# Performance work log

Hardware: AMD Instinct MI355X
Metric: run time of the kernel (lower is better)

The kernel has to match this reference:

```python
import jax, jax.numpy as jnp
import numpy as np

DIST = 3.0
COEFF = 10.0
NEG_SLOPE = 0.3  # keras LeakyReLU default


def _probe_points(dist=DIST):
    # fixed 26 probe offsets on a sphere of radius `dist` (from build())
    angles = np.array(
        [[j * 0.125 - 0.125, i * 0.125 + (j - 1) * 0.0625] for j in range(3) for i in range(8)]
        + [[-0.25, 0.0], [0.25, 0.0]],
        dtype=np.float32,
    ) * (2.0 * np.pi)
    a, b = angles[:, 0], angles[:, 1]
    pts = np.stack([np.sin(a), np.cos(a) * np.cos(b), np.cos(a) * np.sin(b)], axis=-1) * dist
    return jnp.asarray(pts, dtype=jnp.float32)  # (26, 3)


def setup_inputs() -> dict:
    key = jax.random.key(0)
    k1, k2, k3 = jax.random.split(key, 3)
    B, n, f = 2, 1024, 3
    m, out_feats, num_convs = 26, 6, 5
    points = jax.random.normal(k1, (B, n, 3 + f), dtype=jnp.float32)
    # per-conv Dense(m*f -> out_feats) weights/bias, stacked over num_convs
    W = jax.random.normal(k2, (num_convs, m * f, out_feats), dtype=jnp.float32) * 0.1
    b = jax.random.normal(k3, (num_convs, out_feats), dtype=jnp.float32) * 0.1
    return {"points": points, "W": W, "b": b}


def reference(points, W, b):
    B, n, df = points.shape
    d = 3
    f = df - d
    probes = _probe_points()              # (m, d)
    m = probes.shape[0]
    coords = points[..., :d]              # (B, n, d) -> centers too (l = n)
    feats = points[..., d:]               # (B, n, f)
    centers = coords
    # probes per center: (B, l, m, d)
    probes_per_center = centers[:, :, None, :] + probes[None, None, :, :]
    # delta: (B, l, m, n, d)
    delta = coords[:, None, None, :, :] - probes_per_center[:, :, :, None, :]
    sq = jnp.sum(delta * delta, axis=-1)  # (B, l, m, n)
    wgt = COEFF / (sq + COEFF)            # inverse-distance weights
    # weighted feature sum: (B, l, m, f), averaged over n
    wf = jnp.einsum('blmn,bnf->blmf', wgt, feats) / n
    x = wf.reshape(B, n, m * f)           # (B, l, m*f)
    # num_convs parallel Dense + LeakyReLU (Dropout is identity at inference)
    h = jnp.einsum('blx,kxo->blko', x, W) + b[None, None, :, :]
    h = jnp.where(h > 0, h, NEG_SLOPE * h)
    convs = h.reshape(B, n, -1)           # (B, n, num_convs*out_feats)
    return jnp.concatenate([centers, convs], axis=-1)  # (B, n, 3 + 30)
```

## Files before the change

kernel.cpp:

```cpp
#include <hip/hip_runtime.h>


#define NPTS   1024
#define COEFF  10.0f
#define NEG    0.3f

typedef float  v2f __attribute__((ext_vector_type(2)));
typedef __fp16 h2  __attribute__((ext_vector_type(2)));

#define CA 4.24264068f
#define CY 3.91968890f
#define CZ 1.62358830f

constexpr int M0[14] = {0,5, 1,4, 2,3, 7,6, 8,12, 10,14, 24,25};
constexpr int M1[12] = {16,19, 17,18, 20,23, 21,22, 9,13, 11,15};

__device__ __forceinline__ v2f vfma(float c, v2f a, v2f b) {
#if __has_builtin(__builtin_elementwise_fma)
  return __builtin_elementwise_fma(v2f{c, c}, a, b);
#else
  return v2f{fmaf(c, a.x, b.x), fmaf(c, a.y, b.y)};
#endif
}

#define DPP_STEP(x, ctrl, rm, bm, bc)                                        \
  x += __int_as_float(__builtin_amdgcn_update_dpp(                           \
      0, __float_as_int(x), ctrl, rm, bm, bc))

__device__ __forceinline__ float wave_sum_to_lane63(float x) {
  DPP_STEP(x, 0x111, 0xf, 0xf, true);
  DPP_STEP(x, 0x112, 0xf, 0xf, true);
  DPP_STEP(x, 0x114, 0xf, 0xe, false);
  DPP_STEP(x, 0x118, 0xf, 0xc, false);
  DPP_STEP(x, 0x142, 0xa, 0xf, false);
  DPP_STEP(x, 0x143, 0xc, 0xf, false);
  return x;
}

template <int HALF>
__device__ __forceinline__ void tgen(v2f dx, v2f dy, v2f dz, v2f base, v2f* t) {
  if constexpr (HALF == 0) {
    const v2f rx = vfma( CA, dx, base);
    const v2f sA = vfma( CZ, dz, rx);
    const v2f sB = vfma(-CZ, dz, rx);
    const v2f sC = vfma(-CY, dz, rx);
    const v2f sD = vfma( CY, dz, rx);
    t[0]  = vfma(-CY, dy, sA);   t[1]  = vfma( CY, dy, sA);
    t[2]  = vfma(-CY, dy, sB);   t[3]  = vfma( CY, dy, sB);
    t[4]  = vfma(-CZ, dy, sC);   t[5]  = vfma( CZ, dy, sC);
    t[6]  = vfma(-CZ, dy, sD);   t[7]  = vfma( CZ, dy, sD);
    t[8]  = vfma(-6.f, dy, base); t[9]  = vfma( 6.f, dy, base);
    t[10] = vfma(-6.f, dz, base); t[11] = vfma( 6.f, dz, base);
    t[12] = vfma( 6.f, dx, base); t[13] = vfma(-6.f, dx, base);
  } else {
    const v2f rx = vfma(-CA, dx, base);
    const v2f sA = vfma(-CZ, dz, rx);
    const v2f sB = vfma(-CY, dz, rx);
    const v2f sC = vfma( CZ, dz, rx);
    const v2f sD = vfma( CY, dz, rx);
    const v2f u = dy + dz, v = dy - dz;
    t[0]  = vfma(-CY, dy, sA);   t[1]  = vfma( CY, dy, sA);
    t[2]  = vfma(-CZ, dy, sB);   t[3]  = vfma( CZ, dy, sB);
    t[4]  = vfma( CY, dy, sC);   t[5]  = vfma(-CY, dy, sC);
    t[6]  = vfma( CZ, dy, sD);   t[7]  = vfma(-CZ, dy, sD);
    t[8]  = vfma(-CA, u, base);  t[9]  = vfma( CA, u, base);
    t[10] = vfma( CA, v, base);  t[11] = vfma(-CA, v, base);
  }
}

template <int HALF>
__device__ void run_main(const float* __restrict__ batch, int lane,
                         float cx, float cy, float cz, float* acc) {
  constexpr int NP = HALF ? 12 : 14;
  for (int it = 0; it < NPTS / 128; ++it) {
    const float* prowA = batch + (it * 128 + lane) * 6;
    const float* prowB = prowA + 64 * 6;
    const float2 a0 = *reinterpret_cast<const float2*>(prowA);
    const float2 a1 = *reinterpret_cast<const float2*>(prowA + 2);
    const float2 a2 = *reinterpret_cast<const float2*>(prowA + 4);
    const float2 b0 = *reinterpret_cast<const float2*>(prowB);
    const float2 b1 = *reinterpret_cast<const float2*>(prowB + 2);
    const float2 b2 = *reinterpret_cast<const float2*>(prowB + 4);

    const v2f dx = v2f{a0.x, b0.x} - cx;
    const v2f dy = v2f{a0.y, b0.y} - cy;
    const v2f dz = v2f{a1.x, b1.x} - cz;
    v2f base = vfma(1.f, dz * dz, v2f{19.f, 19.f});
    base = __builtin_elementwise_fma(dy, dy, base);
    base = __builtin_elementwise_fma(dx, dx, base);

    v2f t[NP];
    tgen<HALF>(dx, dy, dz, base, t);

    const h2 f0p = __builtin_amdgcn_cvt_pkrtz(a1.y, b1.y);
    const h2 f1p = __builtin_amdgcn_cvt_pkrtz(a2.x, b2.x);
    const h2 f2p = __builtin_amdgcn_cvt_pkrtz(a2.y, b2.y);

    #pragma unroll
    for (int j = 0; j < NP; ++j) {
      const float r  = __builtin_amdgcn_rcpf(t[j].x * t[j].y);
      const h2 wp = __builtin_amdgcn_cvt_pkrtz(t[j].y * r, t[j].x * r);
      acc[j * 3 + 0] = __builtin_amdgcn_fdot2(wp, f0p, acc[j * 3 + 0], false);
      acc[j * 3 + 1] = __builtin_amdgcn_fdot2(wp, f1p, acc[j * 3 + 1], false);
      acc[j * 3 + 2] = __builtin_amdgcn_fdot2(wp, f2p, acc[j * 3 + 2], false);
    }
  }
}

template <int HALF>
__device__ __forceinline__ void reduce_store(float* acc, int lane, float* sx) {
  constexpr int NP = HALF ? 12 : 14;
  #pragma unroll
  for (int j = 0; j < NP * 3; ++j)
    acc[j] = wave_sum_to_lane63(acc[j]);
  if (lane == 63) {
    #pragma unroll
    for (int j = 0; j < NP; ++j) {
      const int m = HALF ? M1[j] : M0[j];
      sx[m * 3 + 0] = acc[j * 3 + 0];
      sx[m * 3 + 1] = acc[j * 3 + 1];
      sx[m * 3 + 2] = acc[j * 3 + 2];
    }
  }
}

__global__ __launch_bounds__(256, 4) void crossconv_kernel(
    const float* __restrict__ points,
    const float* __restrict__ W,
    const float* __restrict__ bias,
    float* __restrict__ out)
{
    __shared__ __align__(16) float sx[2][80];

    const int tid    = threadIdx.x;
    const int lane   = tid & 63;
    const int w      = tid >> 6;
    const int cLocal = w >> 1;
    const int half   = w & 1;
    const int G      = blockIdx.x * 2 + cLocal;

    const float* batch = points + (G >> 10) * (NPTS * 6);
    const float* crow  = points + G * 6;
    const float  cx = crow[0], cy = crow[1], cz = crow[2];

    float acc[42];
    #pragma unroll
    for (int j = 0; j < 42; ++j) acc[j] = 0.f;

    if (half == 0) run_main<0>(batch, lane, cx, cy, cz, acc);
    else           run_main<1>(batch, lane, cx, cy, cz, acc);

    if (half == 0) reduce_store<0>(acc, lane, sx[cLocal]);
    else           reduce_store<1>(acc, lane, sx[cLocal]);
    __syncthreads();

    if (half == 0) {
      const float scale = COEFF / (float)NPTS;
      float* orow = out + G * 33;
      if (lane < 30) {
        const int k = lane / 6, o = lane % 6;
        const float* Wk = W + k * (78 * 6) + o;
        float h0 = 0.f, h1 = 0.f, h2_ = 0.f, h3 = 0.f;
        const float4* sxv = reinterpret_cast<const float4*>(sx[cLocal]);
        #pragma unroll
        for (int t4 = 0; t4 < 19; ++t4) {
          const float4 v = sxv[t4];
          h0  = fmaf(v.x, Wk[(t4 * 4 + 0) * 6], h0);
          h1  = fmaf(v.y, Wk[(t4 * 4 + 1) * 6], h1);
          h2_ = fmaf(v.z, Wk[(t4 * 4 + 2) * 6], h2_);
          h3  = fmaf(v.w, Wk[(t4 * 4 + 3) * 6], h3);
        }
        const float2 vt = *reinterpret_cast<const float2*>(&sx[cLocal][76]);
        h0 = fmaf(vt.x, Wk[76 * 6], h0);
        h1 = fmaf(vt.y, Wk[77 * 6], h1);
        const float dot = (h0 + h2_) + (h1 + h3);
        float h = fmaf(dot, scale, bias[lane]);
        h = (h > 0.f) ? h : NEG * h;
        orow[3 + lane] = h;
      } else if (lane < 33) {
        orow[lane - 30] = (lane == 30) ? cx : ((lane == 31) ? cy : cz);
      }
    }
}

extern "C" void kernel_launch(void* const* d_in, const int* in_sizes, int n_in,
                              void* d_out, int out_size, void* d_ws, size_t ws_size,
                              hipStream_t stream) {
    const float* points = (const float*)d_in[0];
    const float* W      = (const float*)d_in[1];
    const float* bias   = (const float*)d_in[2];
    float* out          = (float*)d_out;
    crossconv_kernel<<<1024, 256, 0, stream>>>(points, W, bias, out);
}
```

Measured before the change: 23.69 us.

## Batch reciprocals across probes, force packed FP32 asm, and reduce in packed fp16

Replaces the per-probe reciprocal with a batched product trick, so one v_rcp serves four probe pairs (eight weights) at the cost of extra multiplies. The probe-distance FMAs are now inline-asm v_pk_fma_f32/v_pk_add_f32 with neg modifiers, so they are guaranteed to issue as packed ops. The final cross-lane DPP reduction converts accumulator pairs to packed fp16 and sums them as h2, halving the DPP steps. Risks: products of up to eight t values may overflow or lose precision in fp32, and summing 64 lanes in fp16 cuts reduction accuracy.

Measured after the change: 23.82 us. Within noise of the previous version (+0.5%).

```diff
diff --git a/kernel.cpp b/kernel.cpp
--- a/kernel.cpp
+++ b/kernel.cpp
@@ -15,63 +15,75 @@
 constexpr int M0[14] = {0,5, 1,4, 2,3, 7,6, 8,12, 10,14, 24,25};
 constexpr int M1[12] = {16,19, 17,18, 20,23, 21,22, 9,13, 11,15};
 
-__device__ __forceinline__ v2f vfma(float c, v2f a, v2f b) {
-#if __has_builtin(__builtin_elementwise_fma)
-  return __builtin_elementwise_fma(v2f{c, c}, a, b);
-#else
-  return v2f{fmaf(c, a.x, b.x), fmaf(c, a.y, b.y)};
-#endif
-}
-
-#define DPP_STEP(x, ctrl, rm, bm, bc)                                        \
+__device__ __forceinline__ v2f pk_fma(v2f a, v2f b, v2f c) {
+  v2f d;
+  asm("v_pk_fma_f32 %0, %1, %2, %3" : "=v"(d) : "v"(a), "v"(b), "v"(c));
+  return d;
+}
+__device__ __forceinline__ v2f pk_fma_n(v2f a, v2f b, v2f c) {
+  v2f d;
+  asm("v_pk_fma_f32 %0, %1, %2, %3 neg_lo:[1,0,0] neg_hi:[1,0,0]"
+      : "=v"(d) : "v"(a), "v"(b), "v"(c));
+  return d;
+}
+__device__ __forceinline__ v2f pk_add(v2f a, v2f b) {
+  v2f d;
+  asm("v_pk_add_f32 %0, %1, %2" : "=v"(d) : "v"(a), "v"(b));
+  return d;
+}
+__device__ __forceinline__ v2f pk_sub(v2f a, v2f b) {
+  v2f d;
+  asm("v_pk_add_f32 %0, %1, %2 neg_lo:[0,1] neg_hi:[0,1]"
+      : "=v"(d) : "v"(a), "v"(b));
+  return d;
+}
+
+#define DPP_F32(x, ctrl, rm, bm, bc)                                         \
   x += __int_as_float(__builtin_amdgcn_update_dpp(                           \
       0, __float_as_int(x), ctrl, rm, bm, bc))
 
-__device__ __forceinline__ float wave_sum_to_lane63(float x) {
-  DPP_STEP(x, 0x111, 0xf, 0xf, true);
-  DPP_STEP(x, 0x112, 0xf, 0xf, true);
-  DPP_STEP(x, 0x114, 0xf, 0xe, false);
-  DPP_STEP(x, 0x118, 0xf, 0xc, false);
-  DPP_STEP(x, 0x142, 0xa, 0xf, false);
-  DPP_STEP(x, 0x143, 0xc, 0xf, false);
+#define DPP_H2(x, ctrl, rm, bm, bc)                                          \
+  x = x + __builtin_bit_cast(h2, __builtin_amdgcn_update_dpp(                \
+      0, __builtin_bit_cast(int, x), ctrl, rm, bm, bc))
+
+__device__ __forceinline__ h2 h2_wave_sum_to_lane63(h2 x) {
+  DPP_H2(x, 0x111, 0xf, 0xf, true);
+  DPP_H2(x, 0x112, 0xf, 0xf, true);
+  DPP_H2(x, 0x114, 0xf, 0xe, false);
+  DPP_H2(x, 0x118, 0xf, 0xc, false);
+  DPP_H2(x, 0x142, 0xa, 0xf, false);
+  DPP_H2(x, 0x143, 0xc, 0xf, false);
   return x;
 }
 
-template <int HALF>
-__device__ __forceinline__ void tgen(v2f dx, v2f dy, v2f dz, v2f base, v2f* t) {
-  if constexpr (HALF == 0) {
-    const v2f rx = vfma( CA, dx, base);
-    const v2f sA = vfma( CZ, dz, rx);
-    const v2f sB = vfma(-CZ, dz, rx);
-    const v2f sC = vfma(-CY, dz, rx);
-    const v2f sD = vfma( CY, dz, rx);
-    t[0]  = vfma(-CY, dy, sA);   t[1]  = vfma( CY, dy, sA);
-    t[2]  = vfma(-CY, dy, sB);   t[3]  = vfma( CY, dy, sB);
-    t[4]  = vfma(-CZ, dy, sC);   t[5]  = vfma( CZ, dy, sC);
-    t[6]  = vfma(-CZ, dy, sD);   t[7]  = vfma( CZ, dy, sD);
-    t[8]  = vfma(-6.f, dy, base); t[9]  = vfma( 6.f, dy, base);
-    t[10] = vfma(-6.f, dz, base); t[11] = vfma( 6.f, dz, base);
-    t[12] = vfma( 6.f, dx, base); t[13] = vfma(-6.f, dx, base);
-  } else {
-    const v2f rx = vfma(-CA, dx, base);
-    const v2f sA = vfma(-CZ, dz, rx);
-    const v2f sB = vfma(-CY, dz, rx);
-    const v2f sC = vfma( CZ, dz, rx);
-    const v2f sD = vfma( CY, dz, rx);
-    const v2f u = dy + dz, v = dy - dz;
-    t[0]  = vfma(-CY, dy, sA);   t[1]  = vfma( CY, dy, sA);
-    t[2]  = vfma(-CZ, dy, sB);   t[3]  = vfma( CZ, dy, sB);
-    t[4]  = vfma( CY, dy, sC);   t[5]  = vfma(-CY, dy, sC);
-    t[6]  = vfma( CZ, dy, sD);   t[7]  = vfma(-CZ, dy, sD);
-    t[8]  = vfma(-CA, u, base);  t[9]  = vfma( CA, u, base);
-    t[10] = vfma( CA, v, base);  t[11] = vfma(-CA, v, base);
-  }
+__device__ __forceinline__ void rcp8_cvt(const v2f* t, h2* wp) {
+  const float p0 = t[0].x * t[0].y, p1 = t[1].x * t[1].y;
+  const float p2 = t[2].x * t[2].y, p3 = t[3].x * t[3].y;
+  const float q01 = p0 * p1, q23 = p2 * p3;
+  const float r   = __builtin_amdgcn_rcpf(q01 * q23);
+  const float r01 = q23 * r, r23 = q01 * r;
+  const float i0 = p1 * r01, i1 = p0 * r01;
+  const float i2 = p3 * r23, i3 = p2 * r23;
+  wp[0] = __builtin_amdgcn_cvt_pkrtz(t[0].y * i0, t[0].x * i0);
+  wp[1] = __builtin_amdgcn_cvt_pkrtz(t[1].y * i1, t[1].x * i1);
+  wp[2] = __builtin_amdgcn_cvt_pkrtz(t[2].y * i2, t[2].x * i2);
+  wp[3] = __builtin_amdgcn_cvt_pkrtz(t[3].y * i3, t[3].x * i3);
+}
+__device__ __forceinline__ void rcp4_cvt(const v2f* t, h2* wp) {
+  const float p0 = t[0].x * t[0].y, p1 = t[1].x * t[1].y;
+  const float r  = __builtin_amdgcn_rcpf(p0 * p1);
+  const float i0 = p1 * r, i1 = p0 * r;
+  wp[0] = __builtin_amdgcn_cvt_pkrtz(t[0].y * i0, t[0].x * i0);
+  wp[1] = __builtin_amdgcn_cvt_pkrtz(t[1].y * i1, t[1].x * i1);
 }
 
 template <int HALF>
 __device__ void run_main(const float* __restrict__ batch, int lane,
-                         float cx, float cy, float cz, float* acc) {
+                         v2f cxp, v2f cyp, v2f czp, float* acc) {
   constexpr int NP = HALF ? 12 : 14;
+  const v2f kCA = {CA, CA}, kCY = {CY, CY}, kCZ = {CZ, CZ};
+  const v2f k6 = {6.f, 6.f}, k19 = {19.f, 19.f};
+
   for (int it = 0; it < NPTS / 128; ++it) {
     const float* prowA = batch + (it * 128 + lane) * 6;
     const float* prowB = prowA + 64 * 6;
@@ -82,15 +94,47 @@
     const float2 b1 = *reinterpret_cast<const float2*>(prowB + 2);
     const float2 b2 = *reinterpret_cast<const float2*>(prowB + 4);
 
-    const v2f dx = v2f{a0.x, b0.x} - cx;
-    const v2f dy = v2f{a0.y, b0.y} - cy;
-    const v2f dz = v2f{a1.x, b1.x} - cz;
-    v2f base = vfma(1.f, dz * dz, v2f{19.f, 19.f});
-    base = __builtin_elementwise_fma(dy, dy, base);
-    base = __builtin_elementwise_fma(dx, dx, base);
+    const v2f dx = pk_sub(v2f{a0.x, b0.x}, cxp);
+    const v2f dy = pk_sub(v2f{a0.y, b0.y}, cyp);
+    const v2f dz = pk_sub(v2f{a1.x, b1.x}, czp);
+    v2f base = pk_fma(dz, dz, k19);
+    base = pk_fma(dy, dy, base);
+    base = pk_fma(dx, dx, base);
 
     v2f t[NP];
-    tgen<HALF>(dx, dy, dz, base, t);
+    if constexpr (HALF == 0) {
+      const v2f rx = pk_fma(kCA, dx, base);
+      const v2f sA = pk_fma  (kCZ, dz, rx);
+      const v2f sB = pk_fma_n(kCZ, dz, rx);
+      const v2f sC = pk_fma_n(kCY, dz, rx);
+      const v2f sD = pk_fma  (kCY, dz, rx);
+      t[0]  = pk_fma_n(kCY, dy, sA);  t[1]  = pk_fma(kCY, dy, sA);
+      t[2]  = pk_fma_n(kCY, dy, sB);  t[3]  = pk_fma(kCY, dy, sB);
+      t[4]  = pk_fma_n(kCZ, dy, sC);  t[5]  = pk_fma(kCZ, dy, sC);
+      t[6]  = pk_fma_n(kCZ, dy, sD);  t[7]  = pk_fma(kCZ, dy, sD);
+      t[8]  = pk_fma_n(k6, dy, base); t[9]  = pk_fma(k6, dy, base);
+      t[10] = pk_fma_n(k6, dz, base); t[11] = pk_fma(k6, dz, base);
+      t[12] = pk_fma  (k6, dx, base); t[13] = pk_fma_n(k6, dx, base);
+    } else {
+      const v2f rx = pk_fma_n(kCA, dx, base);
+      const v2f sA = pk_fma_n(kCZ, dz, rx);
+      const v2f sB = pk_fma_n(kCY, dz, rx);
+      const v2f sC = pk_fma  (kCZ, dz, rx);
+      const v2f sD = pk_fma  (kCY, dz, rx);
+      const v2f u = pk_add(dy, dz), v = pk_sub(dy, dz);
+      t[0]  = pk_fma_n(kCY, dy, sA);  t[1]  = pk_fma(kCY, dy, sA);
+      t[2]  = pk_fma_n(kCZ, dy, sB);  t[3]  = pk_fma(kCZ, dy, sB);
+      t[4]  = pk_fma  (kCY, dy, sC);  t[5]  = pk_fma_n(kCY, dy, sC);
+      t[6]  = pk_fma  (kCZ, dy, sD);  t[7]  = pk_fma_n(kCZ, dy, sD);
+      t[8]  = pk_fma_n(kCA, u, base); t[9]  = pk_fma(kCA, u, base);
+      t[10] = pk_fma  (kCA, v, base); t[11] = pk_fma_n(kCA, v, base);
+    }
+
+    h2 wp[NP];
+    rcp8_cvt(t + 0, wp + 0);
+    rcp8_cvt(t + 4, wp + 4);
+    rcp8_cvt(t + 8, wp + 8);
+    if constexpr (NP == 14) rcp4_cvt(t + 12, wp + 12);
 
     const h2 f0p = __builtin_amdgcn_cvt_pkrtz(a1.y, b1.y);
     const h2 f1p = __builtin_amdgcn_cvt_pkrtz(a2.x, b2.x);
@@ -98,11 +142,9 @@
 
     #pragma unroll
     for (int j = 0; j < NP; ++j) {
-      const float r  = __builtin_amdgcn_rcpf(t[j].x * t[j].y);
-      const h2 wp = __builtin_amdgcn_cvt_pkrtz(t[j].y * r, t[j].x * r);
-      acc[j * 3 + 0] = __builtin_amdgcn_fdot2(wp, f0p, acc[j * 3 + 0], false);
-      acc[j * 3 + 1] = __builtin_amdgcn_fdot2(wp, f1p, acc[j * 3 + 1], false);
-      acc[j * 3 + 2] = __builtin_amdgcn_fdot2(wp, f2p, acc[j * 3 + 2], false);
+      acc[j * 3 + 0] = __builtin_amdgcn_fdot2(wp[j], f0p, acc[j * 3 + 0], false);
+      acc[j * 3 + 1] = __builtin_amdgcn_fdot2(wp[j], f1p, acc[j * 3 + 1], false);
+      acc[j * 3 + 2] = __builtin_amdgcn_fdot2(wp[j], f2p, acc[j * 3 + 2], false);
     }
   }
 }
@@ -110,16 +152,22 @@
 template <int HALF>
 __device__ __forceinline__ void reduce_store(float* acc, int lane, float* sx) {
   constexpr int NP = HALF ? 12 : 14;
+  constexpr int NH = NP * 3 / 2;
+  h2 red[NH];
   #pragma unroll
-  for (int j = 0; j < NP * 3; ++j)
-    acc[j] = wave_sum_to_lane63(acc[j]);
+  for (int p = 0; p < NH; ++p)
+    red[p] = __builtin_amdgcn_cvt_pkrtz(acc[2 * p], acc[2 * p + 1]);
+  #pragma unroll
+  for (int p = 0; p < NH; ++p)
+    red[p] = h2_wave_sum_to_lane63(red[p]);
   if (lane == 63) {
     #pragma unroll
-    for (int j = 0; j < NP; ++j) {
-      const int m = HALF ? M1[j] : M0[j];
-      sx[m * 3 + 0] = acc[j * 3 + 0];
-      sx[m * 3 + 1] = acc[j * 3 + 1];
-      sx[m * 3 + 2] = acc[j * 3 + 2];
+    for (int p = 0; p < NH; ++p) {
+      const int a0 = 2 * p, a1 = 2 * p + 1;
+      const int m0 = (HALF ? M1[a0 / 3] : M0[a0 / 3]);
+      const int m1 = (HALF ? M1[a1 / 3] : M0[a1 / 3]);
+      sx[m0 * 3 + a0 % 3] = (float)red[p].x;
+      sx[m1 * 3 + a1 % 3] = (float)red[p].y;
     }
   }
 }
@@ -142,13 +190,14 @@
     const float* batch = points + (G >> 10) * (NPTS * 6);
     const float* crow  = points + G * 6;
     const float  cx = crow[0], cy = crow[1], cz = crow[2];
+    const v2f cxp = {cx, cx}, cyp = {cy, cy}, czp = {cz, cz};
 
     float acc[42];
     #pragma unroll
     for (int j = 0; j < 42; ++j) acc[j] = 0.f;
 
-    if (half == 0) run_main<0>(batch, lane, cx, cy, cz, acc);
-    else           run_main<1>(batch, lane, cx, cy, cz, acc);
+    if (half == 0) run_main<0>(batch, lane, cxp, cyp, czp, acc);
+    else           run_main<1>(batch, lane, cxp, cyp, czp, acc);
 
     if (half == 0) reduce_store<0>(acc, lane, sx[cLocal]);
     else           reduce_store<1>(acc, lane, sx[cLocal]);
```
